# Optimization experiments

Measured on AMD Instinct MI355X. Metric: run time of the kernel, lower is better.

## Reference

```python
import jax, jax.numpy as jnp
import numpy as np

N_NODES = 100000
E_MAIN = 1600000   # '_E' edges
E_ACC = 200000     # 'account' edges
D = 128            # dim_in == dim_out
FE = 4             # edge feature width (hard-coded in source)


def setup_inputs() -> dict:
    key = jax.random.key(0)
    ks = jax.random.split(key, 14)
    inp = {
        "feats": jax.random.normal(ks[0], (N_NODES, D), jnp.float32),
        "edge_feats": jax.random.normal(ks[1], (E_MAIN, FE), jnp.float32),
        "src_E": jax.random.randint(ks[2], (E_MAIN,), 0, N_NODES),
        "dst_E": jax.random.randint(ks[3], (E_MAIN,), 0, N_NODES),
        "src_acc": jax.random.randint(ks[4], (E_ACC,), 0, N_NODES),
        "dst_acc": jax.random.randint(ks[5], (E_ACC,), 0, N_NODES),
        "W_skip": jax.random.normal(ks[6], (D, D), jnp.float32) * 0.05,
        "b_skip": jnp.zeros((D,), jnp.float32),
        "W_msg": jax.random.normal(ks[7], (D, D), jnp.float32) * 0.05,
        "b_msg": jnp.zeros((D,), jnp.float32),
        "W_edge": jax.random.normal(ks[8], (D, FE), jnp.float32) * 0.5,
        "b_edge": jax.random.normal(ks[9], (D,), jnp.float32) * 0.1,
        "W_att": jax.random.normal(ks[10], (1, FE), jnp.float32) * 0.5,
        "b_att": jax.random.normal(ks[11], (1,), jnp.float32) * 0.1,
    }
    return inp


def reference(feats, edge_feats, src_E, dst_E, src_acc, dst_acc,
              W_skip, b_skip, W_msg, b_msg, W_edge, b_edge, W_att, b_att):
    n = feats.shape[0]
    # symmetric-ish degree norm from '_E' source rows (matches self.norm)
    deg = jax.ops.segment_sum(jnp.ones(src_E.shape[0], feats.dtype), src_E,
                              num_segments=n)
    deg_safe = jnp.where(deg > 0, deg, 1.0)
    norm = jnp.where(deg > 0, deg_safe ** -0.5, 0.0)  # [N]
    h = feats * norm[:, None]                         # srcdata['h'] == dstdata['h']

    def messages(ef, s, d):
        # per-edge: sigmoid attention * src + transformed edge feat + dst
        att = jax.nn.sigmoid(ef @ W_att.T + b_att)    # [E,1]
        tr = ef @ W_edge.T + b_edge                   # [E,D]
        return att * h[s] + tr + h[d]                 # [E,D]

    agg = jax.ops.segment_sum(messages(edge_feats, src_E, dst_E), dst_E,
                              num_segments=n)
    # 'account' etype gets zero edge features (as in source)
    ef_acc = jnp.zeros((src_acc.shape[0], edge_feats.shape[1]), feats.dtype)
    agg = agg + jax.ops.segment_sum(messages(ef_acc, src_acc, dst_acc), dst_acc,
                                    num_segments=n)

    rst = agg * norm[:, None]
    return rst @ W_msg.T + b_msg + (feats @ W_skip.T + b_skip)
```

## Files before the change

### kernel.cpp

```cpp
#include <hip/hip_runtime.h>
#include <hip/hip_bf16.h>

#define NN 100000
#define NP 100096
#define EM 1600000
#define EA 200000
#define ET (EM + EA)
#define SB 98

#define HC 128
#define CNT_CHUNK 14063
#define DEG_CHUNK 12500
#define PITCHW 25024
#define PITCHB 100096

#define OFF_NORM 0
#define OFF_CNT  (NN)
#define OFF_CUR  (2*NN)
#define OFF_BSUM (3*NN)
#define OFF_WB   (3*NN + 128)
#define OFF_REC  (OFF_WB + 16384)
#define OFF_FB   (OFF_REC + 4*ET)
#define OFF_RB   (OFF_FB + 64*NP)
#define OFF_RANK (OFF_RB + 64*NP)

#define UNP_LO(u) __uint_as_float((u) << 16)
#define UNP_HI(u) __uint_as_float((u) & 0xFFFF0000u)

typedef __attribute__((ext_vector_type(8))) short bf16x8;
typedef __attribute__((ext_vector_type(4))) float f32x4;

static __device__ __forceinline__ unsigned pack_bf16x2(float a, float b) {
  union { __hip_bfloat162 v; unsigned u; } cv;
  cv.v = __float22bfloat162_rn(make_float2(a, b));
  return cv.u;
}

__global__ __launch_bounds__(1024) void k_hist(
    const int* __restrict__ srcE, const int* __restrict__ dstE,
    const int* __restrict__ dstA, const float* __restrict__ feats,
    unsigned* __restrict__ featsb,
    unsigned* __restrict__ hist8w, unsigned* __restrict__ deg8w,
    unsigned short* __restrict__ rank16) {
  __shared__ unsigned h[PITCHW];
  int tid = threadIdx.x;
  int bid = blockIdx.x;

  for (int i = bid * 1024 + tid; i < NP * 64; i += 2 * HC * 1024) {
    if (i < NN * 64) {
      float2 f = ((const float2*)feats)[i];
      featsb[i] = pack_bf16x2(f.x, f.y);
    } else {
      featsb[i] = 0u;
    }
  }

  for (int i = tid; i < PITCHW; i += 1024) h[i] = 0u;
  __syncthreads();
  if (bid < HC) {
    int c = bid;
    int e1 = c * CNT_CHUNK + CNT_CHUNK; if (e1 > ET) e1 = ET;
    for (int e = c * CNT_CHUNK + tid; e < e1; e += 1024) {
      int d = (e < EM) ? dstE[e] : dstA[e - EM];
      unsigned sh = 8u * (unsigned)(d & 3);
      unsigned old = atomicAdd(&h[d >> 2], 1u << sh);
      unsigned lr = (old >> sh) & 255u;
      rank16[e] = (unsigned short)(((unsigned)c << 9) | lr);
    }
    __syncthreads();
    unsigned* dst = hist8w + (size_t)c * PITCHW;
    for (int i = tid; i < PITCHW; i += 1024) dst[i] = h[i];
  } else {
    int c = bid - HC;
    int e1 = c * DEG_CHUNK + DEG_CHUNK;
    for (int e = c * DEG_CHUNK + tid; e < e1; e += 1024) {
      int s = srcE[e];
      atomicAdd(&h[s >> 2], 1u << (8u * (unsigned)(s & 3)));
    }
    __syncthreads();
    unsigned* dst = deg8w + (size_t)c * PITCHW;
    for (int i = tid; i < PITCHW; i += 1024) dst[i] = h[i];
  }
}

__global__ __launch_bounds__(256) void k_merge_wt(
    unsigned* __restrict__ hist8w, const unsigned* __restrict__ deg8w,
    unsigned* __restrict__ cnt, float* __restrict__ norm,
    int* __restrict__ bsum,
    const float* __restrict__ Wmsg, const float* __restrict__ Wskip,
    unsigned* __restrict__ Wb) {
  __shared__ int ws4[4];
  int tid = threadIdx.x;
  int i = blockIdx.x * 256 + tid;
  int tot = 0;
  if (i < PITCHW) {
    unsigned t4 = 0;
#pragma unroll 16
    for (int c = 0; c < HC; ++c) {
      unsigned* p = hist8w + (size_t)c * PITCHW + i;
      unsigned w = *p;
      *p = t4;
      t4 += w;
    }
    unsigned d4 = 0;
#pragma unroll 16
    for (int c = 0; c < HC; ++c) d4 += deg8w[(size_t)c * PITCHW + i];
    int n0 = i * 4;
#pragma unroll
    for (int k = 0; k < 4; ++k) {
      unsigned b = (t4 >> (8 * k)) & 255u;
      tot += (int)b;
      if (n0 + k < NN) {
        cnt[n0 + k] = b;
        unsigned dg = (d4 >> (8 * k)) & 255u;
        norm[n0 + k] = dg ? rsqrtf((float)dg) : 0.0f;
      }
    }
  }
  int lane = tid & 63, wid = tid >> 6;
#pragma unroll
  for (int s = 1; s < 64; s <<= 1) tot += __shfl_xor(tot, s, 64);
  if (lane == 0) ws4[wid] = tot;
  __syncthreads();
  if (tid == 0) bsum[blockIdx.x] = ws4[0] + ws4[1] + ws4[2] + ws4[3];

  if (i < 16384) {
    int j = i >> 7, kk = i & 127;
    float a, b;
    if (kk < 64) {
      a = Wmsg[j * 128 + 2 * kk];
      b = Wmsg[j * 128 + 2 * kk + 1];
    } else {
      a = Wskip[j * 128 + 2 * kk - 128];
      b = Wskip[j * 128 + 2 * kk - 127];
    }
    Wb[j * 128 + kk] = pack_bf16x2(a, b);
  }
}

__global__ __launch_bounds__(64) void k_scan2(int* __restrict__ bsum) {
  int lane = threadIdx.x;
  int v0 = (lane < SB) ? bsum[lane] : 0;
  int v1 = (64 + lane < SB) ? bsum[64 + lane] : 0;
  int x0 = v0, x1 = v1;
#pragma unroll
  for (int s = 1; s < 64; s <<= 1) {
    int y = __shfl_up(x0, s, 64); if (lane >= s) x0 += y;
  }
#pragma unroll
  for (int s = 1; s < 64; s <<= 1) {
    int y = __shfl_up(x1, s, 64); if (lane >= s) x1 += y;
  }
  int t0 = __shfl(x0, 63, 64);
  if (lane < SB) bsum[lane] = x0 - v0;
  if (64 + lane < SB) bsum[64 + lane] = t0 + x1 - v1;
}

__global__ __launch_bounds__(1024) void k_scan3(const unsigned* __restrict__ cnt,
                                                const int* __restrict__ bsum,
                                                int* __restrict__ cursor) {
  __shared__ int ws16[16];
  int tid = threadIdx.x, lane = tid & 63, wid = tid >> 6;
  int i = blockIdx.x * 1024 + tid;
  int v = (i < NN) ? (int)cnt[i] : 0;
  int x = v;
#pragma unroll
  for (int s = 1; s < 64; s <<= 1) {
    int y = __shfl_up(x, s, 64); if (lane >= s) x += y;
  }
  if (lane == 63) ws16[wid] = x;
  __syncthreads();
  if (tid == 0) {
    int a = bsum[blockIdx.x];
#pragma unroll
    for (int w = 0; w < 16; ++w) { int t = ws16[w]; ws16[w] = a; a += t; }
  }
  __syncthreads();
  if (i < NN) cursor[i] = ws16[wid] + x - v;
}

__global__ __launch_bounds__(256) void k_fill(
    const int* __restrict__ srcE, const int* __restrict__ dstE,
    const int* __restrict__ srcA, const int* __restrict__ dstA,
    const float* __restrict__ ef, const float* __restrict__ Watt,
    const float* __restrict__ batt, const float* __restrict__ norm,
    const int* __restrict__ cursor, const unsigned char* __restrict__ hist8,
    const unsigned short* __restrict__ rank16,
    uint4* __restrict__ rec) {
  int e = blockIdx.x * 256 + threadIdx.x;
  if (e >= ET) return;
  int s, d;
  float att;
  float4 f;
  if (e < EM) {
    s = srcE[e]; d = dstE[e];
    f = ((const float4*)ef)[e];
    float z = f.x * Watt[0] + f.y * Watt[1] + f.z * Watt[2] + f.w * Watt[3] + batt[0];
    att = 1.0f / (1.0f + __expf(-z));
  } else {
    int ea = e - EM;
    s = srcA[ea]; d = dstA[ea];
    f = make_float4(0.f, 0.f, 0.f, 0.f);
    att = 1.0f / (1.0f + __expf(-batt[0]));
  }
  float c = att * norm[s];
  unsigned rr = rank16[e];
  int slot = cursor[d] + (int)hist8[(size_t)(rr >> 9) * PITCHB + d]
           + (int)(rr & 511u);
  rec[slot] = make_uint4((unsigned)s, __float_as_uint(c),
                         pack_bf16x2(f.x, f.y), pack_bf16x2(f.z, f.w));
}

__global__ __launch_bounds__(256) void k_pull(
    const unsigned* __restrict__ featsb,
    const unsigned* __restrict__ cnt, const int* __restrict__ cursor,
    const float* __restrict__ norm, const uint4* __restrict__ rec,
    const float* __restrict__ Wedge, const float* __restrict__ bedge,
    unsigned* __restrict__ rstb) {
  int lane = threadIdx.x & 63, wid = threadIdx.x >> 6;
  int n = blockIdx.x * 4 + wid;
  if (n >= NP) return;
  if (n >= NN) { rstb[n * 64 + lane] = 0u; return; }

  int beg = __builtin_amdgcn_readfirstlane(cursor[n]);
  int len = __builtin_amdgcn_readfirstlane((int)cnt[n]);
  int end = beg + len;
  float2 acc = make_float2(0.f, 0.f);
  float4 efa = make_float4(0.f, 0.f, 0.f, 0.f);
  int e = beg;
  for (; e + 8 <= end; e += 8) {
    uint4 r0 = rec[e+0], r1 = rec[e+1], r2 = rec[e+2], r3 = rec[e+3];
    uint4 r4 = rec[e+4], r5 = rec[e+5], r6 = rec[e+6], r7 = rec[e+7];
    unsigned u0 = featsb[r0.x * 64 + lane];
    unsigned u1 = featsb[r1.x * 64 + lane];
    unsigned u2 = featsb[r2.x * 64 + lane];
    unsigned u3 = featsb[r3.x * 64 + lane];
    unsigned u4 = featsb[r4.x * 64 + lane];
    unsigned u5 = featsb[r5.x * 64 + lane];
    unsigned u6 = featsb[r6.x * 64 + lane];
    unsigned u7 = featsb[r7.x * 64 + lane];
    float c0 = __uint_as_float(r0.y), c1 = __uint_as_float(r1.y);
    float c2 = __uint_as_float(r2.y), c3 = __uint_as_float(r3.y);
    float c4 = __uint_as_float(r4.y), c5 = __uint_as_float(r5.y);
    float c6 = __uint_as_float(r6.y), c7 = __uint_as_float(r7.y);
    acc.x += c0 * UNP_LO(u0) + c1 * UNP_LO(u1) + c2 * UNP_LO(u2) + c3 * UNP_LO(u3)
           + c4 * UNP_LO(u4) + c5 * UNP_LO(u5) + c6 * UNP_LO(u6) + c7 * UNP_LO(u7);
    acc.y += c0 * UNP_HI(u0) + c1 * UNP_HI(u1) + c2 * UNP_HI(u2) + c3 * UNP_HI(u3)
           + c4 * UNP_HI(u4) + c5 * UNP_HI(u5) + c6 * UNP_HI(u6) + c7 * UNP_HI(u7);
    efa.x += UNP_LO(r0.z) + UNP_LO(r1.z) + UNP_LO(r2.z) + UNP_LO(r3.z)
           + UNP_LO(r4.z) + UNP_LO(r5.z) + UNP_LO(r6.z) + UNP_LO(r7.z);
    efa.y += UNP_HI(r0.z) + UNP_HI(r1.z) + UNP_HI(r2.z) + UNP_HI(r3.z)
           + UNP_HI(r4.z) + UNP_HI(r5.z) + UNP_HI(r6.z) + UNP_HI(r7.z);
    efa.z += UNP_LO(r0.w) + UNP_LO(r1.w) + UNP_LO(r2.w) + UNP_LO(r3.w)
           + UNP_LO(r4.w) + UNP_LO(r5.w) + UNP_LO(r6.w) + UNP_LO(r7.w);
    efa.w += UNP_HI(r0.w) + UNP_HI(r1.w) + UNP_HI(r2.w) + UNP_HI(r3.w)
           + UNP_HI(r4.w) + UNP_HI(r5.w) + UNP_HI(r6.w) + UNP_HI(r7.w);
  }
  for (; e < end; ++e) {
    uint4 r = rec[e];
    unsigned u = featsb[r.x * 64 + lane];
    float c = __uint_as_float(r.y);
    acc.x += c * UNP_LO(u);
    acc.y += c * UNP_HI(u);
    efa.x += UNP_LO(r.z); efa.y += UNP_HI(r.z);
    efa.z += UNP_LO(r.w); efa.w += UNP_HI(r.w);
  }
  float flen = (float)len;
  float nm = norm[n];
  unsigned ud = featsb[n * 64 + lane];
  float fx = UNP_LO(ud), fy = UNP_HI(ud);
  float4 wa = ((const float4*)Wedge)[2 * lane + 0];
  float4 wb = ((const float4*)Wedge)[2 * lane + 1];
  float2 be = ((const float2*)bedge)[lane];
  float tx = wa.x * efa.x + wa.y * efa.y + wa.z * efa.z + wa.w * efa.w;
  float ty = wb.x * efa.x + wb.y * efa.y + wb.z * efa.z + wb.w * efa.w;
  float rx = (acc.x + tx + flen * (be.x + nm * fx)) * nm;
  float ry = (acc.y + ty + flen * (be.y + nm * fy)) * nm;
  rstb[n * 64 + lane] = pack_bf16x2(rx, ry);
}

__global__ __launch_bounds__(256) void k_gemm(
    const unsigned* __restrict__ rstb, const unsigned* __restrict__ featsb,
    const unsigned* __restrict__ Wb,
    const float* __restrict__ bmsg, const float* __restrict__ bskip,
    float* __restrict__ out) {
  int lane = threadIdx.x & 63, wid = threadIdx.x >> 6;
  int quad = lane >> 4, l15 = lane & 15;
  int rowt = blockIdx.x * 128 + wid * 32;
  int m0 = rowt + l15;
  int m1 = m0 + 16;

  f32x4 acc0[8], acc1[8];
#pragma unroll
  for (int ct = 0; ct < 8; ++ct) {
    acc0[ct] = (f32x4){0.f, 0.f, 0.f, 0.f};
    acc1[ct] = (f32x4){0.f, 0.f, 0.f, 0.f};
  }

#pragma unroll
  for (int ks = 0; ks < 8; ++ks) {
    int kb = ks * 32;
    const unsigned* Xsrc = (kb < 128) ? rstb : featsb;
    int off = ((kb & 127) >> 1) + quad * 4;
    bf16x8 a0 = *(const bf16x8*)(Xsrc + m0 * 64 + off);
    bf16x8 a1 = *(const bf16x8*)(Xsrc + m1 * 64 + off);
#pragma unroll
    for (int ct = 0; ct < 8; ++ct) {
      int j = ct * 16 + l15;
      bf16x8 b = *(const bf16x8*)(Wb + j * 128 + (kb >> 1) + quad * 4);
      acc0[ct] = __builtin_amdgcn_mfma_f32_16x16x32_bf16(a0, b, acc0[ct], 0, 0, 0);
      acc1[ct] = __builtin_amdgcn_mfma_f32_16x16x32_bf16(a1, b, acc1[ct], 0, 0, 0);
    }
  }

#pragma unroll
  for (int ct = 0; ct < 8; ++ct) {
    int col = ct * 16 + l15;
    float bia = bmsg[col] + bskip[col];
#pragma unroll
    for (int r = 0; r < 4; ++r) {
      int row0 = rowt + quad * 4 + r;
      if (row0 < NN) out[row0 * 128 + col] = acc0[ct][r] + bia;
      int row1 = row0 + 16;
      if (row1 < NN) out[row1 * 128 + col] = acc1[ct][r] + bia;
    }
  }
}

extern "C" void kernel_launch(void* const* d_in, const int* in_sizes, int n_in,
                              void* d_out, int out_size, void* d_ws, size_t ws_size,
                              hipStream_t stream) {
  const float* feats  = (const float*)d_in[0];
  const float* ef     = (const float*)d_in[1];
  const int*   srcE   = (const int*)d_in[2];
  const int*   dstE   = (const int*)d_in[3];
  const int*   srcA   = (const int*)d_in[4];
  const int*   dstA   = (const int*)d_in[5];
  const float* Wskip  = (const float*)d_in[6];
  const float* bskip  = (const float*)d_in[7];
  const float* Wmsg   = (const float*)d_in[8];
  const float* bmsg   = (const float*)d_in[9];
  const float* Wedge  = (const float*)d_in[10];
  const float* bedge  = (const float*)d_in[11];
  const float* Watt   = (const float*)d_in[12];
  const float* batt   = (const float*)d_in[13];
  float* out = (float*)d_out;
  float* ws  = (float*)d_ws;

  float*          norm   = ws + OFF_NORM;
  unsigned*       cnt    = (unsigned*)(ws + OFF_CNT);
  int*            cursor = (int*)(ws + OFF_CUR);
  int*            bsum   = (int*)(ws + OFF_BSUM);
  unsigned*       Wb     = (unsigned*)(ws + OFF_WB);
  uint4*          rec    = (uint4*)(ws + OFF_REC);
  unsigned*       featsb = (unsigned*)(ws + OFF_FB);
  unsigned*       rstb   = (unsigned*)(ws + OFF_RB);
  unsigned short* rank16 = (unsigned short*)(ws + OFF_RANK);

  unsigned*       hist8w = rstb;
  unsigned*       deg8w  = rstb + (size_t)HC * PITCHW;
  unsigned char*  hist8b = (unsigned char*)hist8w;

  k_hist<<<2 * HC, 1024, 0, stream>>>(srcE, dstE, dstA, feats, featsb,
                                      hist8w, deg8w, rank16);
  k_merge_wt<<<SB, 256, 0, stream>>>(hist8w, deg8w, cnt, norm, bsum,
                                     Wmsg, Wskip, Wb);
  k_scan2<<<1, 64, 0, stream>>>(bsum);
  k_scan3<<<SB, 1024, 0, stream>>>(cnt, bsum, cursor);
  k_fill<<<(ET + 255) / 256, 256, 0, stream>>>(srcE, dstE, srcA, dstA, ef, Watt,
                                               batt, norm, cursor, hist8b,
                                               rank16, rec);
  k_pull<<<NP / 4, 256, 0, stream>>>(featsb, cnt, cursor, norm,
                                     rec, Wedge, bedge, rstb);
  k_gemm<<<NP / 128, 256, 0, stream>>>(rstb, featsb, Wb, bmsg, bskip, out);
}
```

Before: 370.0 us.

## Fuse pull aggregation with MFMA GEMM via LDS and merge scan kernels

The per-node gather/aggregate kernel and the bf16 MFMA GEMM are fused: each wave aggregates 16 nodes, stages the packed bf16 rows in shared memory, then runs the 16-row MFMA tile directly, which removes the rstb round trip through global memory and one launch. The two-stage block-sum scan is folded into the final scan, where each block serially sums the preceding block totals, dropping another launch. In exchange, each wave processes 16 nodes serially, so the gather has much less parallelism (1564 blocks instead of about 25k). The GEMM tile also shrinks to 16 rows per wave, so weight reuse drops.

```diff
diff --git a/kernel.cpp b/kernel.cpp
--- a/kernel.cpp
+++ b/kernel.cpp
@@ -21,8 +21,8 @@
 #define OFF_WB   (3*NN + 128)
 #define OFF_REC  (OFF_WB + 16384)
 #define OFF_FB   (OFF_REC + 4*ET)
-#define OFF_RB   (OFF_FB + 64*NP)
-#define OFF_RANK (OFF_RB + 64*NP)
+#define OFF_HIST (OFF_FB + 64*NP)
+#define OFF_RANK (OFF_HIST + 2*HC*PITCHW)
 
 #define UNP_LO(u) __uint_as_float((u) << 16)
 #define UNP_HI(u) __uint_as_float((u) & 0xFFFF0000u)
@@ -138,27 +138,9 @@
   }
 }
 
-__global__ __launch_bounds__(64) void k_scan2(int* __restrict__ bsum) {
-  int lane = threadIdx.x;
-  int v0 = (lane < SB) ? bsum[lane] : 0;
-  int v1 = (64 + lane < SB) ? bsum[64 + lane] : 0;
-  int x0 = v0, x1 = v1;
-#pragma unroll
-  for (int s = 1; s < 64; s <<= 1) {
-    int y = __shfl_up(x0, s, 64); if (lane >= s) x0 += y;
-  }
-#pragma unroll
-  for (int s = 1; s < 64; s <<= 1) {
-    int y = __shfl_up(x1, s, 64); if (lane >= s) x1 += y;
-  }
-  int t0 = __shfl(x0, 63, 64);
-  if (lane < SB) bsum[lane] = x0 - v0;
-  if (64 + lane < SB) bsum[64 + lane] = t0 + x1 - v1;
-}
-
-__global__ __launch_bounds__(1024) void k_scan3(const unsigned* __restrict__ cnt,
-                                                const int* __restrict__ bsum,
-                                                int* __restrict__ cursor) {
+__global__ __launch_bounds__(1024) void k_scan(const unsigned* __restrict__ cnt,
+                                               const int* __restrict__ bsum,
+                                               int* __restrict__ cursor) {
   __shared__ int ws16[16];
   int tid = threadIdx.x, lane = tid & 63, wid = tid >> 6;
   int i = blockIdx.x * 1024 + tid;
@@ -171,7 +153,8 @@
   if (lane == 63) ws16[wid] = x;
   __syncthreads();
   if (tid == 0) {
-    int a = bsum[blockIdx.x];
+    int a = 0;
+    for (int b = 0; b < blockIdx.x; ++b) a += bsum[b];
 #pragma unroll
     for (int w = 0; w < 16; ++w) { int t = ws16[w]; ws16[w] = a; a += t; }
   }
@@ -211,105 +194,105 @@
                          pack_bf16x2(f.x, f.y), pack_bf16x2(f.z, f.w));
 }
 
-__global__ __launch_bounds__(256) void k_pull(
+__global__ __launch_bounds__(256) void k_pullg(
     const unsigned* __restrict__ featsb,
     const unsigned* __restrict__ cnt, const int* __restrict__ cursor,
     const float* __restrict__ norm, const uint4* __restrict__ rec,
     const float* __restrict__ Wedge, const float* __restrict__ bedge,
-    unsigned* __restrict__ rstb) {
+    const unsigned* __restrict__ Wb,
+    const float* __restrict__ bmsg, const float* __restrict__ bskip,
+    float* __restrict__ out) {
+  __shared__ unsigned lA[4][16 * 68];
   int lane = threadIdx.x & 63, wid = threadIdx.x >> 6;
-  int n = blockIdx.x * 4 + wid;
-  if (n >= NP) return;
-  if (n >= NN) { rstb[n * 64 + lane] = 0u; return; }
-
-  int beg = __builtin_amdgcn_readfirstlane(cursor[n]);
-  int len = __builtin_amdgcn_readfirstlane((int)cnt[n]);
-  int end = beg + len;
-  float2 acc = make_float2(0.f, 0.f);
-  float4 efa = make_float4(0.f, 0.f, 0.f, 0.f);
-  int e = beg;
-  for (; e + 8 <= end; e += 8) {
-    uint4 r0 = rec[e+0], r1 = rec[e+1], r2 = rec[e+2], r3 = rec[e+3];
-    uint4 r4 = rec[e+4], r5 = rec[e+5], r6 = rec[e+6], r7 = rec[e+7];
-    unsigned u0 = featsb[r0.x * 64 + lane];
-    unsigned u1 = featsb[r1.x * 64 + lane];
-    unsigned u2 = featsb[r2.x * 64 + lane];
-    unsigned u3 = featsb[r3.x * 64 + lane];
-    unsigned u4 = featsb[r4.x * 64 + lane];
-    unsigned u5 = featsb[r5.x * 64 + lane];
-    unsigned u6 = featsb[r6.x * 64 + lane];
-    unsigned u7 = featsb[r7.x * 64 + lane];
-    float c0 = __uint_as_float(r0.y), c1 = __uint_as_float(r1.y);
-    float c2 = __uint_as_float(r2.y), c3 = __uint_as_float(r3.y);
-    float c4 = __uint_as_float(r4.y), c5 = __uint_as_float(r5.y);
-    float c6 = __uint_as_float(r6.y), c7 = __uint_as_float(r7.y);
-    acc.x += c0 * UNP_LO(u0) + c1 * UNP_LO(u1) + c2 * UNP_LO(u2) + c3 * UNP_LO(u3)
-           + c4 * UNP_LO(u4) + c5 * UNP_LO(u5) + c6 * UNP_LO(u6) + c7 * UNP_LO(u7);
-    acc.y += c0 * UNP_HI(u0) + c1 * UNP_HI(u1) + c2 * UNP_HI(u2) + c3 * UNP_HI(u3)
-           + c4 * UNP_HI(u4) + c5 * UNP_HI(u5) + c6 * UNP_HI(u6) + c7 * UNP_HI(u7);
-    efa.x += UNP_LO(r0.z) + UNP_LO(r1.z) + UNP_LO(r2.z) + UNP_LO(r3.z)
-           + UNP_LO(r4.z) + UNP_LO(r5.z) + UNP_LO(r6.z) + UNP_LO(r7.z);
-    efa.y += UNP_HI(r0.z) + UNP_HI(r1.z) + UNP_HI(r2.z) + UNP_HI(r3.z)
-           + UNP_HI(r4.z) + UNP_HI(r5.z) + UNP_HI(r6.z) + UNP_HI(r7.z);
-    efa.z += UNP_LO(r0.w) + UNP_LO(r1.w) + UNP_LO(r2.w) + UNP_LO(r3.w)
-           + UNP_LO(r4.w) + UNP_LO(r5.w) + UNP_LO(r6.w) + UNP_LO(r7.w);
-    efa.w += UNP_HI(r0.w) + UNP_HI(r1.w) + UNP_HI(r2.w) + UNP_HI(r3.w)
-           + UNP_HI(r4.w) + UNP_HI(r5.w) + UNP_HI(r6.w) + UNP_HI(r7.w);
-  }
-  for (; e < end; ++e) {
-    uint4 r = rec[e];
-    unsigned u = featsb[r.x * 64 + lane];
-    float c = __uint_as_float(r.y);
-    acc.x += c * UNP_LO(u);
-    acc.y += c * UNP_HI(u);
-    efa.x += UNP_LO(r.z); efa.y += UNP_HI(r.z);
-    efa.z += UNP_LO(r.w); efa.w += UNP_HI(r.w);
-  }
-  float flen = (float)len;
-  float nm = norm[n];
-  unsigned ud = featsb[n * 64 + lane];
-  float fx = UNP_LO(ud), fy = UNP_HI(ud);
+  int rowt = blockIdx.x * 64 + wid * 16;
+  unsigned* lw = &lA[wid][0];
+
   float4 wa = ((const float4*)Wedge)[2 * lane + 0];
   float4 wb = ((const float4*)Wedge)[2 * lane + 1];
   float2 be = ((const float2*)bedge)[lane];
-  float tx = wa.x * efa.x + wa.y * efa.y + wa.z * efa.z + wa.w * efa.w;
-  float ty = wb.x * efa.x + wb.y * efa.y + wb.z * efa.z + wb.w * efa.w;
-  float rx = (acc.x + tx + flen * (be.x + nm * fx)) * nm;
-  float ry = (acc.y + ty + flen * (be.y + nm * fy)) * nm;
-  rstb[n * 64 + lane] = pack_bf16x2(rx, ry);
-}
-
-__global__ __launch_bounds__(256) void k_gemm(
-    const unsigned* __restrict__ rstb, const unsigned* __restrict__ featsb,
-    const unsigned* __restrict__ Wb,
-    const float* __restrict__ bmsg, const float* __restrict__ bskip,
-    float* __restrict__ out) {
-  int lane = threadIdx.x & 63, wid = threadIdx.x >> 6;
+
+  for (int i = 0; i < 16; ++i) {
+    int n = rowt + i;
+    float rx = 0.f, ry = 0.f;
+    if (n < NN) {
+      int beg = __builtin_amdgcn_readfirstlane(cursor[n]);
+      int len = __builtin_amdgcn_readfirstlane((int)cnt[n]);
+      int end = beg + len;
+      float2 acc = make_float2(0.f, 0.f);
+      float4 efa = make_float4(0.f, 0.f, 0.f, 0.f);
+      int e = beg;
+      for (; e + 8 <= end; e += 8) {
+        uint4 r0 = rec[e+0], r1 = rec[e+1], r2 = rec[e+2], r3 = rec[e+3];
+        uint4 r4 = rec[e+4], r5 = rec[e+5], r6 = rec[e+6], r7 = rec[e+7];
+        unsigned u0 = featsb[r0.x * 64 + lane];
+        unsigned u1 = featsb[r1.x * 64 + lane];
+        unsigned u2 = featsb[r2.x * 64 + lane];
+        unsigned u3 = featsb[r3.x * 64 + lane];
+        unsigned u4 = featsb[r4.x * 64 + lane];
+        unsigned u5 = featsb[r5.x * 64 + lane];
+        unsigned u6 = featsb[r6.x * 64 + lane];
+        unsigned u7 = featsb[r7.x * 64 + lane];
+        float c0 = __uint_as_float(r0.y), c1 = __uint_as_float(r1.y);
+        float c2 = __uint_as_float(r2.y), c3 = __uint_as_float(r3.y);
+        float c4 = __uint_as_float(r4.y), c5 = __uint_as_float(r5.y);
+        float c6 = __uint_as_float(r6.y), c7 = __uint_as_float(r7.y);
+        acc.x += c0 * UNP_LO(u0) + c1 * UNP_LO(u1) + c2 * UNP_LO(u2)
+               + c3 * UNP_LO(u3) + c4 * UNP_LO(u4) + c5 * UNP_LO(u5)
+               + c6 * UNP_LO(u6) + c7 * UNP_LO(u7);
+        acc.y += c0 * UNP_HI(u0) + c1 * UNP_HI(u1) + c2 * UNP_HI(u2)
+               + c3 * UNP_HI(u3) + c4 * UNP_HI(u4) + c5 * UNP_HI(u5)
+               + c6 * UNP_HI(u6) + c7 * UNP_HI(u7);
+        efa.x += UNP_LO(r0.z) + UNP_LO(r1.z) + UNP_LO(r2.z) + UNP_LO(r3.z)
+               + UNP_LO(r4.z) + UNP_LO(r5.z) + UNP_LO(r6.z) + UNP_LO(r7.z);
+        efa.y += UNP_HI(r0.z) + UNP_HI(r1.z) + UNP_HI(r2.z) + UNP_HI(r3.z)
+               + UNP_HI(r4.z) + UNP_HI(r5.z) + UNP_HI(r6.z) + UNP_HI(r7.z);
+        efa.z += UNP_LO(r0.w) + UNP_LO(r1.w) + UNP_LO(r2.w) + UNP_LO(r3.w)
+               + UNP_LO(r4.w) + UNP_LO(r5.w) + UNP_LO(r6.w) + UNP_LO(r7.w);
+        efa.w += UNP_HI(r0.w) + UNP_HI(r1.w) + UNP_HI(r2.w) + UNP_HI(r3.w)
+               + UNP_HI(r4.w) + UNP_HI(r5.w) + UNP_HI(r6.w) + UNP_HI(r7.w);
+      }
+      for (; e < end; ++e) {
+        uint4 r = rec[e];
+        unsigned u = featsb[r.x * 64 + lane];
+        float c = __uint_as_float(r.y);
+        acc.x += c * UNP_LO(u);
+        acc.y += c * UNP_HI(u);
+        efa.x += UNP_LO(r.z); efa.y += UNP_HI(r.z);
+        efa.z += UNP_LO(r.w); efa.w += UNP_HI(r.w);
+      }
+      float flen = (float)len;
+      float nm = norm[n];
+      unsigned ud = featsb[n * 64 + lane];
+      float fx = UNP_LO(ud), fy = UNP_HI(ud);
+      float tx = wa.x * efa.x + wa.y * efa.y + wa.z * efa.z + wa.w * efa.w;
+      float ty = wb.x * efa.x + wb.y * efa.y + wb.z * efa.z + wb.w * efa.w;
+      rx = (acc.x + tx + flen * (be.x + nm * fx)) * nm;
+      ry = (acc.y + ty + flen * (be.y + nm * fy)) * nm;
+    }
+    lw[i * 68 + lane] = pack_bf16x2(rx, ry);
+  }
+
   int quad = lane >> 4, l15 = lane & 15;
-  int rowt = blockIdx.x * 128 + wid * 32;
   int m0 = rowt + l15;
-  int m1 = m0 + 16;
-
-  f32x4 acc0[8], acc1[8];
-#pragma unroll
-  for (int ct = 0; ct < 8; ++ct) {
-    acc0[ct] = (f32x4){0.f, 0.f, 0.f, 0.f};
-    acc1[ct] = (f32x4){0.f, 0.f, 0.f, 0.f};
-  }
+
+  f32x4 acc0[8];
+#pragma unroll
+  for (int ct = 0; ct < 8; ++ct) acc0[ct] = (f32x4){0.f, 0.f, 0.f, 0.f};
 
 #pragma unroll
   for (int ks = 0; ks < 8; ++ks) {
     int kb = ks * 32;
-    const unsigned* Xsrc = (kb < 128) ? rstb : featsb;
-    int off = ((kb & 127) >> 1) + quad * 4;
-    bf16x8 a0 = *(const bf16x8*)(Xsrc + m0 * 64 + off);
-    bf16x8 a1 = *(const bf16x8*)(Xsrc + m1 * 64 + off);
+    bf16x8 a0;
+    if (ks < 4) {
+      a0 = *(const bf16x8*)(lw + l15 * 68 + ks * 16 + quad * 4);
+    } else {
+      a0 = *(const bf16x8*)(featsb + (size_t)m0 * 64 + (ks - 4) * 16 + quad * 4);
+    }
 #pragma unroll
     for (int ct = 0; ct < 8; ++ct) {
       int j = ct * 16 + l15;
       bf16x8 b = *(const bf16x8*)(Wb + j * 128 + (kb >> 1) + quad * 4);
       acc0[ct] = __builtin_amdgcn_mfma_f32_16x16x32_bf16(a0, b, acc0[ct], 0, 0, 0);
-      acc1[ct] = __builtin_amdgcn_mfma_f32_16x16x32_bf16(a1, b, acc1[ct], 0, 0, 0);
     }
   }
 
@@ -321,8 +304,6 @@
     for (int r = 0; r < 4; ++r) {
       int row0 = rowt + quad * 4 + r;
       if (row0 < NN) out[row0 * 128 + col] = acc0[ct][r] + bia;
-      int row1 = row0 + 16;
-      if (row1 < NN) out[row1 * 128 + col] = acc1[ct][r] + bia;
     }
   }
 }
@@ -354,23 +335,20 @@
   unsigned*       Wb     = (unsigned*)(ws + OFF_WB);
   uint4*          rec    = (uint4*)(ws + OFF_REC);
   unsigned*       featsb = (unsigned*)(ws + OFF_FB);
-  unsigned*       rstb   = (unsigned*)(ws + OFF_RB);
   unsigned short* rank16 = (unsigned short*)(ws + OFF_RANK);
 
-  unsigned*       hist8w = rstb;
-  unsigned*       deg8w  = rstb + (size_t)HC * PITCHW;
+  unsigned*       hist8w = (unsigned*)(ws + OFF_HIST);
+  unsigned*       deg8w  = hist8w + (size_t)HC * PITCHW;
   unsigned char*  hist8b = (unsigned char*)hist8w;
 
   k_hist<<<2 * HC, 1024, 0, stream>>>(srcE, dstE, dstA, feats, featsb,
                                       hist8w, deg8w, rank16);
   k_merge_wt<<<SB, 256, 0, stream>>>(hist8w, deg8w, cnt, norm, bsum,
                                      Wmsg, Wskip, Wb);
-  k_scan2<<<1, 64, 0, stream>>>(bsum);
-  k_scan3<<<SB, 1024, 0, stream>>>(cnt, bsum, cursor);
+  k_scan<<<SB, 1024, 0, stream>>>(cnt, bsum, cursor);
   k_fill<<<(ET + 255) / 256, 256, 0, stream>>>(srcE, dstE, srcA, dstA, ef, Watt,
                                                batt, norm, cursor, hist8b,
                                                rank16, rec);
-  k_pull<<<NP / 4, 256, 0, stream>>>(featsb, cnt, cursor, norm,
-                                     rec, Wedge, bedge, rstb);
-  k_gemm<<<NP / 128, 256, 0, stream>>>(rstb, featsb, Wb, bmsg, bskip, out);
-}
+  k_pullg<<<NP / 64, 256, 0, stream>>>(featsb, cnt, cursor, norm, rec,
+                                       Wedge, bedge, Wb, bmsg, bskip, out);
+}
```

Measured after the change: 403.7 us. 1.09x slower.

## Stage per-chunk histogram in LDS for fill and fold block-sum scan into scan kernel

Applied to the files above, without the earlier changes.

The fill kernel now launches one block per half of each edge chunk. Each block loads that chunk's 8-bit per-destination histogram row (about 100KB) into shared memory, so the byte-granular global gather becomes an LDS read. The separate single-block scan2 launch is removed, and each scan block sums the preceding block totals serially in thread 0. The trade-off is a large LDS footprint per block, which limits occupancy to about one block per CU, plus only 256 blocks for 1.8M edges.

```diff
diff --git a/kernel.cpp b/kernel.cpp
--- a/kernel.cpp
+++ b/kernel.cpp
@@ -138,27 +138,9 @@
   }
 }
 
-__global__ __launch_bounds__(64) void k_scan2(int* __restrict__ bsum) {
-  int lane = threadIdx.x;
-  int v0 = (lane < SB) ? bsum[lane] : 0;
-  int v1 = (64 + lane < SB) ? bsum[64 + lane] : 0;
-  int x0 = v0, x1 = v1;
-#pragma unroll
-  for (int s = 1; s < 64; s <<= 1) {
-    int y = __shfl_up(x0, s, 64); if (lane >= s) x0 += y;
-  }
-#pragma unroll
-  for (int s = 1; s < 64; s <<= 1) {
-    int y = __shfl_up(x1, s, 64); if (lane >= s) x1 += y;
-  }
-  int t0 = __shfl(x0, 63, 64);
-  if (lane < SB) bsum[lane] = x0 - v0;
-  if (64 + lane < SB) bsum[64 + lane] = t0 + x1 - v1;
-}
-
-__global__ __launch_bounds__(1024) void k_scan3(const unsigned* __restrict__ cnt,
-                                                const int* __restrict__ bsum,
-                                                int* __restrict__ cursor) {
+__global__ __launch_bounds__(1024) void k_scan(const unsigned* __restrict__ cnt,
+                                               const int* __restrict__ bsum,
+                                               int* __restrict__ cursor) {
   __shared__ int ws16[16];
   int tid = threadIdx.x, lane = tid & 63, wid = tid >> 6;
   int i = blockIdx.x * 1024 + tid;
@@ -171,7 +153,8 @@
   if (lane == 63) ws16[wid] = x;
   __syncthreads();
   if (tid == 0) {
-    int a = bsum[blockIdx.x];
+    int a = 0;
+    for (int b = 0; b < blockIdx.x; ++b) a += bsum[b];
 #pragma unroll
     for (int w = 0; w < 16; ++w) { int t = ws16[w]; ws16[w] = a; a += t; }
   }
@@ -179,36 +162,54 @@
   if (i < NN) cursor[i] = ws16[wid] + x - v;
 }
 
-__global__ __launch_bounds__(256) void k_fill(
+__global__ __launch_bounds__(1024) void k_fill(
     const int* __restrict__ srcE, const int* __restrict__ dstE,
     const int* __restrict__ srcA, const int* __restrict__ dstA,
     const float* __restrict__ ef, const float* __restrict__ Watt,
     const float* __restrict__ batt, const float* __restrict__ norm,
-    const int* __restrict__ cursor, const unsigned char* __restrict__ hist8,
+    const int* __restrict__ cursor, const unsigned* __restrict__ hist8w,
     const unsigned short* __restrict__ rank16,
     uint4* __restrict__ rec) {
-  int e = blockIdx.x * 256 + threadIdx.x;
-  if (e >= ET) return;
-  int s, d;
-  float att;
-  float4 f;
-  if (e < EM) {
-    s = srcE[e]; d = dstE[e];
-    f = ((const float4*)ef)[e];
-    float z = f.x * Watt[0] + f.y * Watt[1] + f.z * Watt[2] + f.w * Watt[3] + batt[0];
-    att = 1.0f / (1.0f + __expf(-z));
-  } else {
-    int ea = e - EM;
-    s = srcA[ea]; d = dstA[ea];
-    f = make_float4(0.f, 0.f, 0.f, 0.f);
-    att = 1.0f / (1.0f + __expf(-batt[0]));
-  }
-  float c = att * norm[s];
-  unsigned rr = rank16[e];
-  int slot = cursor[d] + (int)hist8[(size_t)(rr >> 9) * PITCHB + d]
-           + (int)(rr & 511u);
-  rec[slot] = make_uint4((unsigned)s, __float_as_uint(c),
-                         pack_bf16x2(f.x, f.y), pack_bf16x2(f.z, f.w));
+  __shared__ unsigned sl[PITCHW];
+  int tid = threadIdx.x;
+  int bid = blockIdx.x;
+  int c = bid >> 1, half = bid & 1;
+
+  const unsigned* src = hist8w + (size_t)c * PITCHW;
+  for (int i = tid; i < PITCHW; i += 1024) sl[i] = src[i];
+  __syncthreads();
+
+  int e0 = c * CNT_CHUNK;
+  int e1 = e0 + CNT_CHUNK; if (e1 > ET) e1 = ET;
+  int mid = e0 + ((e1 - e0 + 1) >> 1);
+  int lo = half ? mid : e0;
+  int hi = half ? e1 : mid;
+
+  float w0 = Watt[0], w1 = Watt[1], w2 = Watt[2], w3 = Watt[3], b0 = batt[0];
+  float attA = 1.0f / (1.0f + __expf(-b0));
+
+  for (int e = lo + tid; e < hi; e += 1024) {
+    int s, d;
+    float att;
+    float4 f;
+    if (e < EM) {
+      s = srcE[e]; d = dstE[e];
+      f = ((const float4*)ef)[e];
+      float z = f.x * w0 + f.y * w1 + f.z * w2 + f.w * w3 + b0;
+      att = 1.0f / (1.0f + __expf(-z));
+    } else {
+      int ea = e - EM;
+      s = srcA[ea]; d = dstA[ea];
+      f = make_float4(0.f, 0.f, 0.f, 0.f);
+      att = attA;
+    }
+    float cf = att * norm[s];
+    unsigned rr = rank16[e];
+    unsigned base = (sl[d >> 2] >> (8u * (unsigned)(d & 3))) & 255u;
+    int slot = cursor[d] + (int)base + (int)(rr & 511u);
+    rec[slot] = make_uint4((unsigned)s, __float_as_uint(cf),
+                           pack_bf16x2(f.x, f.y), pack_bf16x2(f.z, f.w));
+  }
 }
 
 __global__ __launch_bounds__(256) void k_pull(
@@ -359,17 +360,15 @@
 
   unsigned*       hist8w = rstb;
   unsigned*       deg8w  = rstb + (size_t)HC * PITCHW;
-  unsigned char*  hist8b = (unsigned char*)hist8w;
 
   k_hist<<<2 * HC, 1024, 0, stream>>>(srcE, dstE, dstA, feats, featsb,
                                       hist8w, deg8w, rank16);
   k_merge_wt<<<SB, 256, 0, stream>>>(hist8w, deg8w, cnt, norm, bsum,
                                      Wmsg, Wskip, Wb);
-  k_scan2<<<1, 64, 0, stream>>>(bsum);
-  k_scan3<<<SB, 1024, 0, stream>>>(cnt, bsum, cursor);
-  k_fill<<<(ET + 255) / 256, 256, 0, stream>>>(srcE, dstE, srcA, dstA, ef, Watt,
-                                               batt, norm, cursor, hist8b,
-                                               rank16, rec);
+  k_scan<<<SB, 1024, 0, stream>>>(cnt, bsum, cursor);
+  k_fill<<<2 * HC, 1024, 0, stream>>>(srcE, dstE, srcA, dstA, ef, Watt,
+                                      batt, norm, cursor, hist8w,
+                                      rank16, rec);
   k_pull<<<NP / 4, 256, 0, stream>>>(featsb, cnt, cursor, norm,
                                      rec, Wedge, bedge, rstb);
   k_gemm<<<NP / 128, 256, 0, stream>>>(rstb, featsb, Wb, bmsg, bskip, out);
```

Result: no change. 376.6 us (+1.8%).
